# Kernel tuning notes

Measured on AMD Instinct MI355X. Metric: run time of the kernel, lower is better.

Reference implementation:

```python
import jax, jax.numpy as jnp
import numpy as np

CIN, COUT, KH, KW = 128, 256, 3, 3

def setup_inputs() -> dict:
    key = jax.random.key(0)
    kx, kw = jax.random.split(key)
    x = jax.random.normal(kx, (32, CIN, 56, 56), dtype=jnp.float32)
    # kaiming normal, fan_in mode, relu gain: std = sqrt(2 / fan_in)
    fan_in = CIN * KH * KW
    weight = jax.random.normal(kw, (COUT, CIN, KH, KW), dtype=jnp.float32) * jnp.sqrt(2.0 / fan_in)
    bias = jnp.zeros((COUT,), dtype=jnp.float32)
    return {"x": x, "weight": weight, "bias": bias}

def reference(x, weight, bias):
    # VALID 2D cross-correlation (matches torch conv semantics of the manual loop)
    y = jax.lax.conv_general_dilated(
        x, weight,
        window_strides=(1, 1),
        padding="VALID",
        dimension_numbers=("NCHW", "OIHW", "NCHW"),
    )
    return y + bias[None, :, None, None]
```

## Files before the change

### kernel.cpp

```cpp
#include <hip/hip_runtime.h>
#include <hip/hip_bf16.h>

#define CIN 128
#define COUT 256
#define H 56
#define W 56
#define OH 54
#define OW 54

typedef __attribute__((ext_vector_type(8))) short short8;
typedef __attribute__((ext_vector_type(4))) float floatx4;

typedef __attribute__((address_space(3))) unsigned int  lds_u32;
typedef const __attribute__((address_space(1))) unsigned int glb_u32;

static __device__ __forceinline__ unsigned short f2bf(float f) {
  unsigned int u = __builtin_bit_cast(unsigned int, f);
  u += 0x7fffu + ((u >> 16) & 1u);
  return (unsigned short)(u >> 16);
}

__global__ void repack_w(const float* __restrict__ w, unsigned short* __restrict__ w2) {
  int idx = blockIdx.x * 256 + threadIdx.x;
  if (idx >= COUT * CIN * 9) return;
  int kw = idx % 3, t1 = idx / 3;
  int kh = t1 % 3, t2 = t1 / 3;
  int ci = t2 % CIN;
  int co = t2 / CIN;
  int c8 = ci >> 3, j = ci & 7;
  w2[((((kh * 3 + kw) * 16 + c8) * COUT + co) * 8) + j] = f2bf(w[idx]);
}

__global__ __launch_bounds__(256) void repack_x(const float* __restrict__ x,
                                                unsigned short* __restrict__ xb) {
  __shared__ float xt[56][129];
  const int h = blockIdx.x;
  const int n = blockIdx.y;
  const float* src = x + (size_t)n * CIN * (H * W) + h * W;
  #pragma unroll
  for (int r = 0; r < 28; ++r) {
    int idx = r * 256 + threadIdx.x;
    int ci = idx / 56, iw = idx % 56;
    xt[iw][ci] = src[ci * (H * W) + iw];
  }
  __syncthreads();
  unsigned short* dst = xb + ((size_t)n * H + h) * 896 * 8;
  #pragma unroll
  for (int r = 0; r < 4; ++r) {
    int g = r * 256 + threadIdx.x;
    if (g < 896) {
      int iw = g >> 4, c16 = g & 15;
      short8 v;
      #pragma unroll
      for (int j = 0; j < 8; ++j)
        v[j] = (short)f2bf(xt[iw][c16 * 8 + j]);
      int gp = iw * 16 + (c16 ^ (iw & 7));
      *reinterpret_cast<short8*>(&dst[gp * 8]) = v;
    }
  }
}

__global__ __launch_bounds__(512, 2) void conv2(
    const unsigned short* __restrict__ xb, const unsigned short* __restrict__ w2,
    const float* __restrict__ bias, float* __restrict__ out) {
  __shared__ alignas(16) unsigned short xs[3744 * 8];

  const int f = blockIdx.x;
  const int swz = (f & 7) * 108 + (f >> 3);
  const int ohp = swz % 27;
  const int n   = swz / 27;
  const int oh0 = ohp * 2;
  const int tid = threadIdx.x;
  const int wid  = tid >> 6;
  const int lane = tid & 63;

  {
    const unsigned short* src = xb + ((size_t)n * H + oh0) * 896 * 8;
    #pragma unroll
    for (int i = 0; i < 7; ++i) {
      int idx = (wid * 7 + i) * 64;
      __builtin_amdgcn_global_load_lds(
          (glb_u32*)(src + (size_t)(idx + lane) * 8),
          (lds_u32*)(&xs[idx * 8]), 16, 0, 0);
    }
  }
  asm volatile("s_waitcnt vmcnt(0)" ::: "memory");
  __syncthreads();

  const int wm   = wid >> 1;
  const int wn   = wid & 1;
  const int l16  = lane & 15;
  const int cig  = lane >> 4;

  const int co_base = wm * 64;
  const int oh = oh0 + wn;

  const unsigned short* wbase = w2 + ((size_t)(cig * COUT + co_base + l16)) * 8;
  const int bwn = wn * 896 * 8;
  int ib[3], x7[3];
  #pragma unroll
  for (int kw = 0; kw < 3; ++kw) {
    ib[kw] = (l16 + kw) * 16 * 8;
    x7[kw] = (l16 + kw) & 7;
  }

  floatx4 acc[4][4];
  #pragma unroll
  for (int m = 0; m < 4; ++m)
    #pragma unroll
    for (int nr = 0; nr < 4; ++nr)
      acc[m][nr] = (floatx4){0.f, 0.f, 0.f, 0.f};

  short8 areg[2][4], breg[2][4];

#define STEP_LOAD(s, slot)                                                      \
  {                                                                             \
    const int kh_ = (s) / 12, ch_ = ((s) / 3) & 3, kw_ = (s) % 3;               \
    const unsigned short* wp_ =                                                 \
        wbase + (size_t)(((kh_ * 3 + kw_) * 16 + ch_ * 4) * COUT) * 8;          \
    areg[slot][0] = *reinterpret_cast<const short8*>(wp_);                      \
    areg[slot][1] = *reinterpret_cast<const short8*>(wp_ + 128);                \
    areg[slot][2] = *reinterpret_cast<const short8*>(wp_ + 256);                \
    areg[slot][3] = *reinterpret_cast<const short8*>(wp_ + 384);                \
    const int c16x_ = (ch_ * 4 + cig) ^ x7[kw_];                                \
    const int boff_ = bwn + kh_ * (896 * 8) + ib[kw_] + c16x_ * 8;              \
    breg[slot][0] = *reinterpret_cast<const short8*>(&xs[boff_]);               \
    breg[slot][1] = *reinterpret_cast<const short8*>(&xs[boff_ + 2048]);        \
    breg[slot][2] = *reinterpret_cast<const short8*>(&xs[boff_ + 4096]);        \
    breg[slot][3] = *reinterpret_cast<const short8*>(&xs[boff_ + 6144]);        \
  }

  STEP_LOAD(0, 0);
  #pragma unroll
  for (int s = 0; s < 36; ++s) {
    if (s < 35) STEP_LOAD(s + 1, (s + 1) & 1);
    __builtin_amdgcn_sched_barrier(0);
    __builtin_amdgcn_s_setprio(1);
    #pragma unroll
    for (int m = 0; m < 4; ++m)
      #pragma unroll
      for (int nr = 0; nr < 4; ++nr)
        acc[m][nr] = __builtin_amdgcn_mfma_f32_16x16x32_bf16(
            areg[s & 1][m], breg[s & 1][nr], acc[m][nr], 0, 0, 0);
    __builtin_amdgcn_s_setprio(0);
  }
#undef STEP_LOAD

  const int rowd = cig * 4;
  #pragma unroll
  for (int m = 0; m < 4; ++m) {
    #pragma unroll
    for (int reg = 0; reg < 4; ++reg) {
      int co = co_base + m * 16 + rowd + reg;
      float bv = bias[co];
      float* op = out + (((size_t)n * COUT + co) * OH + oh) * OW;
      #pragma unroll
      for (int nr = 0; nr < 4; ++nr) {
        int ow = nr * 16 + l16;
        if (ow < OW) op[ow] = acc[m][nr][reg] + bv;
      }
    }
  }
}

#define CSTR 136
#define IWP 66

__global__ __launch_bounds__(512, 4) void conv_fb(
    const float* __restrict__ x, const unsigned short* __restrict__ w2,
    const float* __restrict__ bias, float* __restrict__ out) {
  __shared__ alignas(16) unsigned short xsf[4 * IWP * CSTR];

  const int ohp = blockIdx.x;
  const int n   = blockIdx.y;
  const int oh0 = ohp * 2;
  const int tid = threadIdx.x;

  {
    short8 zz = {0, 0, 0, 0, 0, 0, 0, 0};
    for (int i = tid; i < 4 * 10 * 17; i += 512) {
      int r = i / 170, rem = i % 170;
      int iw = 56 + rem / 17, g = rem % 17;
      *reinterpret_cast<short8*>(&xsf[(r * IWP + iw) * CSTR + g * 8]) = zz;
    }
  }
  for (int s = tid; s < 3584; s += 512) {
    int iw = s % 56;
    int t  = s / 56;
    int c8 = t & 15, r = t >> 4;
    const float* xp = x + (size_t)n * CIN * (H * W) + (oh0 + r) * W + iw;
    short8 v;
    #pragma unroll
    for (int j = 0; j < 8; ++j)
      v[j] = (short)f2bf(xp[(size_t)(c8 * 8 + j) * (H * W)]);
    *reinterpret_cast<short8*>(&xsf[(r * IWP + iw) * CSTR + c8 * 8]) = v;
  }
  __syncthreads();

  const int wid  = tid >> 6;
  const int lane = tid & 63;
  const int wm   = wid >> 1;
  const int wn   = wid & 1;
  const int l16  = lane & 15;
  const int cig  = lane >> 4;

  const int co_base = wm * 64;
  const int oh = oh0 + wn;

  floatx4 acc[4][4];
  #pragma unroll
  for (int m = 0; m < 4; ++m)
    #pragma unroll
    for (int nr = 0; nr < 4; ++nr)
      acc[m][nr] = (floatx4){0.f, 0.f, 0.f, 0.f};

  for (int kh = 0; kh < 3; ++kh) {
    const int row = wn + kh;
    #pragma unroll
    for (int ch = 0; ch < 4; ++ch) {
      const int bbase = (row * IWP + l16) * CSTR + ch * 32 + cig * 8;
      #pragma unroll
      for (int kw = 0; kw < 3; ++kw) {
        const unsigned short* wp =
            w2 + ((size_t)(((kh * 3 + kw) * 16 + (ch * 4 + cig)) * COUT + co_base + l16)) * 8;
        short8 a[4];
        #pragma unroll
        for (int m = 0; m < 4; ++m)
          a[m] = *reinterpret_cast<const short8*>(wp + m * 16 * 8);
        short8 b[4];
        #pragma unroll
        for (int nr = 0; nr < 4; ++nr)
          b[nr] = *reinterpret_cast<const short8*>(&xsf[bbase + (nr * 16 + kw) * CSTR]);
        #pragma unroll
        for (int m = 0; m < 4; ++m)
          #pragma unroll
          for (int nr = 0; nr < 4; ++nr)
            acc[m][nr] = __builtin_amdgcn_mfma_f32_16x16x32_bf16(a[m], b[nr], acc[m][nr], 0, 0, 0);
      }
    }
  }

  const int rowd = cig * 4;
  #pragma unroll
  for (int m = 0; m < 4; ++m) {
    #pragma unroll
    for (int reg = 0; reg < 4; ++reg) {
      int co = co_base + m * 16 + rowd + reg;
      float bv = bias[co];
      float* op = out + (((size_t)n * COUT + co) * OH + oh) * OW;
      #pragma unroll
      for (int nr = 0; nr < 4; ++nr) {
        int ow = nr * 16 + l16;
        if (ow < OW) op[ow] = acc[m][nr][reg] + bv;
      }
    }
  }
}

extern "C" void kernel_launch(void* const* d_in, const int* in_sizes, int n_in,
                              void* d_out, int out_size, void* d_ws, size_t ws_size,
                              hipStream_t stream) {
  (void)in_sizes; (void)n_in; (void)out_size;
  const float* x    = (const float*)d_in[0];
  const float* w    = (const float*)d_in[1];
  const float* bias = (const float*)d_in[2];
  float* out = (float*)d_out;

  const size_t W2_BYTES = (size_t)9 * 16 * COUT * 8 * 2;
  const size_t XB_BYTES = (size_t)32 * H * 896 * 8 * 2;
  unsigned short* w2 = (unsigned short*)d_ws;

  repack_w<<<dim3((COUT * CIN * 9 + 255) / 256), dim3(256), 0, stream>>>(w, w2);

  if (ws_size >= W2_BYTES + XB_BYTES) {
    unsigned short* xb = (unsigned short*)((char*)d_ws + W2_BYTES);
    repack_x<<<dim3(56, 32), dim3(256), 0, stream>>>(x, xb);
    conv2<<<dim3(864), dim3(512), 0, stream>>>(xb, w2, bias, out);
  } else {
    conv_fb<<<dim3(27, 32), dim3(512), 0, stream>>>(x, w2, bias, out);
  }
}
```

Measured before the change: 92.60 us.

## Stage weights through LDS with a three-deep async pipeline in conv kernel

Weights are reordered so each of the 36 reduction steps reads one contiguous 16KB slab. The new conv kernel streams those slabs into a triple-buffered LDS area with async global-to-LDS loads, two steps ahead. Previously each wave loaded its weights straight from global memory into registers. The input-tile load is no longer waited on before the loop, so it overlaps the first weight stages, and bias is loaded up front. The cost is a block barrier every step, more LDS per block (possibly lower occupancy), and reliance on vmcnt ordering being correct.

Measured after the change: 138.4 us. 49.4% more time.

```diff
diff --git a/kernel.cpp b/kernel.cpp
--- a/kernel.cpp
+++ b/kernel.cpp
@@ -20,7 +20,179 @@
   return (unsigned short)(u >> 16);
 }
 
-__global__ void repack_w(const float* __restrict__ w, unsigned short* __restrict__ w2) {
+__global__ void repack_w(const float* __restrict__ w, unsigned short* __restrict__ w3) {
+  int idx = blockIdx.x * 256 + threadIdx.x;
+  if (idx >= COUT * CIN * 9) return;
+  int kw = idx % 3, t1 = idx / 3;
+  int kh = t1 % 3, t2 = t1 / 3;
+  int ci = t2 % CIN;
+  int co = t2 / CIN;
+  int c8 = ci >> 3, j = ci & 7;
+  int ch = c8 >> 2, g = c8 & 3;
+  int s = kh * 12 + ch * 3 + kw;
+  w3[(((s * 4 + g) * COUT + co) * 8) + j] = f2bf(w[idx]);
+}
+
+__global__ __launch_bounds__(256) void repack_x(const float* __restrict__ x,
+                                                unsigned short* __restrict__ xb) {
+  __shared__ float xt[56][129];
+  const int h = blockIdx.x;
+  const int n = blockIdx.y;
+  const float* src = x + (size_t)n * CIN * (H * W) + h * W;
+  #pragma unroll
+  for (int r = 0; r < 28; ++r) {
+    int idx = r * 256 + threadIdx.x;
+    int ci = idx / 56, iw = idx % 56;
+    xt[iw][ci] = src[ci * (H * W) + iw];
+  }
+  __syncthreads();
+  unsigned short* dst = xb + ((size_t)n * H + h) * 896 * 8;
+  #pragma unroll
+  for (int r = 0; r < 4; ++r) {
+    int g = r * 256 + threadIdx.x;
+    if (g < 896) {
+      int iw = g >> 4, c16 = g & 15;
+      short8 v;
+      #pragma unroll
+      for (int j = 0; j < 8; ++j)
+        v[j] = (short)f2bf(xt[iw][c16 * 8 + j]);
+      int gp = iw * 16 + (c16 ^ (iw & 7));
+      *reinterpret_cast<short8*>(&dst[gp * 8]) = v;
+    }
+  }
+}
+
+__global__ __launch_bounds__(512, 2) void conv4(
+    const unsigned short* __restrict__ xb, const unsigned short* __restrict__ w3,
+    const float* __restrict__ bias, float* __restrict__ out) {
+  __shared__ alignas(16) unsigned short xs[3744 * 8];
+  __shared__ alignas(16) unsigned short abuf[3][1024 * 8];
+
+  const int f = blockIdx.x;
+  const int swz = (f & 7) * 108 + (f >> 3);
+  const int ohp = swz % 27;
+  const int n   = swz / 27;
+  const int oh0 = ohp * 2;
+  const int tid = threadIdx.x;
+  const int wid  = tid >> 6;
+  const int lane = tid & 63;
+
+  const int wm   = wid >> 1;
+  const int wn   = wid & 1;
+  const int l16  = lane & 15;
+  const int cig  = lane >> 4;
+  const int co_base = wm * 64;
+  const int oh = oh0 + wn;
+  const int rowd = cig * 4;
+
+  float bv[4][4];
+  #pragma unroll
+  for (int m = 0; m < 4; ++m)
+    #pragma unroll
+    for (int reg = 0; reg < 4; ++reg)
+      bv[m][reg] = bias[co_base + m * 16 + rowd + reg];
+
+  {
+    const unsigned short* src = xb + ((size_t)n * H + oh0) * 896 * 8;
+    #pragma unroll
+    for (int i = 0; i < 7; ++i) {
+      int idx = (wid * 7 + i) * 64;
+      __builtin_amdgcn_global_load_lds(
+          (glb_u32*)(src + (size_t)(idx + lane) * 8),
+          (lds_u32*)(&xs[idx * 8]), 16, 0, 0);
+    }
+  }
+
+#define ASTAGE(t)                                                               \
+  {                                                                             \
+    const unsigned short* asrc_ = w3 + (size_t)(t) * 8192;                      \
+    unsigned short* adst_ = &abuf[(t) % 3][0];                                  \
+    const int b0_ = (wid * 2) * 64;                                             \
+    const int b1_ = (wid * 2 + 1) * 64;                                         \
+    __builtin_amdgcn_global_load_lds((glb_u32*)(asrc_ + (size_t)(b0_ + lane) * 8), \
+                                     (lds_u32*)(adst_ + (size_t)b0_ * 8), 16, 0, 0); \
+    __builtin_amdgcn_global_load_lds((glb_u32*)(asrc_ + (size_t)(b1_ + lane) * 8), \
+                                     (lds_u32*)(adst_ + (size_t)b1_ * 8), 16, 0, 0); \
+  }
+
+  ASTAGE(0);
+  ASTAGE(1);
+  asm volatile("s_waitcnt vmcnt(2)" ::: "memory");
+  __builtin_amdgcn_s_barrier();
+  __builtin_amdgcn_sched_barrier(0);
+
+  const int bwn = wn * 896 * 8;
+  int ib[3], x7[3];
+  #pragma unroll
+  for (int kw = 0; kw < 3; ++kw) {
+    ib[kw] = (l16 + kw) * 128;
+    x7[kw] = (l16 + kw) & 7;
+  }
+  const int aoff = (cig * 256 + co_base + l16) * 8;
+
+  floatx4 acc[4][4];
+  #pragma unroll
+  for (int m = 0; m < 4; ++m)
+    #pragma unroll
+    for (int nr = 0; nr < 4; ++nr)
+      acc[m][nr] = (floatx4){0.f, 0.f, 0.f, 0.f};
+
+  #pragma unroll
+  for (int t = 0; t < 36; ++t) {
+    if (t + 2 < 36) ASTAGE(t + 2);
+
+    const int kh = t / 12, ch = (t / 3) & 3, kw = t % 3;
+    short8 a[4], b[4];
+    const unsigned short* ab = &abuf[t % 3][aoff];
+    a[0] = *reinterpret_cast<const short8*>(ab);
+    a[1] = *reinterpret_cast<const short8*>(ab + 128);
+    a[2] = *reinterpret_cast<const short8*>(ab + 256);
+    a[3] = *reinterpret_cast<const short8*>(ab + 384);
+    const int c16x = (ch * 4 + cig) ^ x7[kw];
+    const int boff = bwn + kh * (896 * 8) + ib[kw] + c16x * 8;
+    b[0] = *reinterpret_cast<const short8*>(&xs[boff]);
+    b[1] = *reinterpret_cast<const short8*>(&xs[boff + 2048]);
+    b[2] = *reinterpret_cast<const short8*>(&xs[boff + 4096]);
+    b[3] = *reinterpret_cast<const short8*>(&xs[boff + 6144]);
+
+    __builtin_amdgcn_sched_barrier(0);
+    __builtin_amdgcn_s_setprio(1);
+    #pragma unroll
+    for (int m = 0; m < 4; ++m)
+      #pragma unroll
+      for (int nr = 0; nr < 4; ++nr)
+        acc[m][nr] = __builtin_amdgcn_mfma_f32_16x16x32_bf16(a[m], b[nr], acc[m][nr], 0, 0, 0);
+    __builtin_amdgcn_s_setprio(0);
+    __builtin_amdgcn_sched_barrier(0);
+
+    if (t < 34)       asm volatile("s_waitcnt vmcnt(2)" ::: "memory");
+    else if (t == 34) asm volatile("s_waitcnt vmcnt(0)" ::: "memory");
+    if (t < 35) {
+      __builtin_amdgcn_s_barrier();
+      __builtin_amdgcn_sched_barrier(0);
+    }
+  }
+#undef ASTAGE
+
+  #pragma unroll
+  for (int m = 0; m < 4; ++m) {
+    #pragma unroll
+    for (int reg = 0; reg < 4; ++reg) {
+      int co = co_base + m * 16 + rowd + reg;
+      float* op = out + (((size_t)n * COUT + co) * OH + oh) * OW;
+      #pragma unroll
+      for (int nr = 0; nr < 4; ++nr) {
+        int ow = nr * 16 + l16;
+        if (ow < OW) op[ow] = acc[m][nr][reg] + bv[m][reg];
+      }
+    }
+  }
+}
+
+#define CSTR 136
+#define IWP 66
+
+__global__ void repack_w_fb(const float* __restrict__ w, unsigned short* __restrict__ w2) {
   int idx = blockIdx.x * 256 + threadIdx.x;
   if (idx >= COUT * CIN * 9) return;
   int kw = idx % 3, t1 = idx / 3;
@@ -30,141 +202,6 @@
   int c8 = ci >> 3, j = ci & 7;
   w2[((((kh * 3 + kw) * 16 + c8) * COUT + co) * 8) + j] = f2bf(w[idx]);
 }
-
-__global__ __launch_bounds__(256) void repack_x(const float* __restrict__ x,
-                                                unsigned short* __restrict__ xb) {
-  __shared__ float xt[56][129];
-  const int h = blockIdx.x;
-  const int n = blockIdx.y;
-  const float* src = x + (size_t)n * CIN * (H * W) + h * W;
-  #pragma unroll
-  for (int r = 0; r < 28; ++r) {
-    int idx = r * 256 + threadIdx.x;
-    int ci = idx / 56, iw = idx % 56;
-    xt[iw][ci] = src[ci * (H * W) + iw];
-  }
-  __syncthreads();
-  unsigned short* dst = xb + ((size_t)n * H + h) * 896 * 8;
-  #pragma unroll
-  for (int r = 0; r < 4; ++r) {
-    int g = r * 256 + threadIdx.x;
-    if (g < 896) {
-      int iw = g >> 4, c16 = g & 15;
-      short8 v;
-      #pragma unroll
-      for (int j = 0; j < 8; ++j)
-        v[j] = (short)f2bf(xt[iw][c16 * 8 + j]);
-      int gp = iw * 16 + (c16 ^ (iw & 7));
-      *reinterpret_cast<short8*>(&dst[gp * 8]) = v;
-    }
-  }
-}
-
-__global__ __launch_bounds__(512, 2) void conv2(
-    const unsigned short* __restrict__ xb, const unsigned short* __restrict__ w2,
-    const float* __restrict__ bias, float* __restrict__ out) {
-  __shared__ alignas(16) unsigned short xs[3744 * 8];
-
-  const int f = blockIdx.x;
-  const int swz = (f & 7) * 108 + (f >> 3);
-  const int ohp = swz % 27;
-  const int n   = swz / 27;
-  const int oh0 = ohp * 2;
-  const int tid = threadIdx.x;
-  const int wid  = tid >> 6;
-  const int lane = tid & 63;
-
-  {
-    const unsigned short* src = xb + ((size_t)n * H + oh0) * 896 * 8;
-    #pragma unroll
-    for (int i = 0; i < 7; ++i) {
-      int idx = (wid * 7 + i) * 64;
-      __builtin_amdgcn_global_load_lds(
-          (glb_u32*)(src + (size_t)(idx + lane) * 8),
-          (lds_u32*)(&xs[idx * 8]), 16, 0, 0);
-    }
-  }
-  asm volatile("s_waitcnt vmcnt(0)" ::: "memory");
-  __syncthreads();
-
-  const int wm   = wid >> 1;
-  const int wn   = wid & 1;
-  const int l16  = lane & 15;
-  const int cig  = lane >> 4;
-
-  const int co_base = wm * 64;
-  const int oh = oh0 + wn;
-
-  const unsigned short* wbase = w2 + ((size_t)(cig * COUT + co_base + l16)) * 8;
-  const int bwn = wn * 896 * 8;
-  int ib[3], x7[3];
-  #pragma unroll
-  for (int kw = 0; kw < 3; ++kw) {
-    ib[kw] = (l16 + kw) * 16 * 8;
-    x7[kw] = (l16 + kw) & 7;
-  }
-
-  floatx4 acc[4][4];
-  #pragma unroll
-  for (int m = 0; m < 4; ++m)
-    #pragma unroll
-    for (int nr = 0; nr < 4; ++nr)
-      acc[m][nr] = (floatx4){0.f, 0.f, 0.f, 0.f};
-
-  short8 areg[2][4], breg[2][4];
-
-#define STEP_LOAD(s, slot)                                                      \
-  {                                                                             \
-    const int kh_ = (s) / 12, ch_ = ((s) / 3) & 3, kw_ = (s) % 3;               \
-    const unsigned short* wp_ =                                                 \
-        wbase + (size_t)(((kh_ * 3 + kw_) * 16 + ch_ * 4) * COUT) * 8;          \
-    areg[slot][0] = *reinterpret_cast<const short8*>(wp_);                      \
-    areg[slot][1] = *reinterpret_cast<const short8*>(wp_ + 128);                \
-    areg[slot][2] = *reinterpret_cast<const short8*>(wp_ + 256);                \
-    areg[slot][3] = *reinterpret_cast<const short8*>(wp_ + 384);                \
-    const int c16x_ = (ch_ * 4 + cig) ^ x7[kw_];                                \
-    const int boff_ = bwn + kh_ * (896 * 8) + ib[kw_] + c16x_ * 8;              \
-    breg[slot][0] = *reinterpret_cast<const short8*>(&xs[boff_]);               \
-    breg[slot][1] = *reinterpret_cast<const short8*>(&xs[boff_ + 2048]);        \
-    breg[slot][2] = *reinterpret_cast<const short8*>(&xs[boff_ + 4096]);        \
-    breg[slot][3] = *reinterpret_cast<const short8*>(&xs[boff_ + 6144]);        \
-  }
-
-  STEP_LOAD(0, 0);
-  #pragma unroll
-  for (int s = 0; s < 36; ++s) {
-    if (s < 35) STEP_LOAD(s + 1, (s + 1) & 1);
-    __builtin_amdgcn_sched_barrier(0);
-    __builtin_amdgcn_s_setprio(1);
-    #pragma unroll
-    for (int m = 0; m < 4; ++m)
-      #pragma unroll
-      for (int nr = 0; nr < 4; ++nr)
-        acc[m][nr] = __builtin_amdgcn_mfma_f32_16x16x32_bf16(
-            areg[s & 1][m], breg[s & 1][nr], acc[m][nr], 0, 0, 0);
-    __builtin_amdgcn_s_setprio(0);
-  }
-#undef STEP_LOAD
-
-  const int rowd = cig * 4;
-  #pragma unroll
-  for (int m = 0; m < 4; ++m) {
-    #pragma unroll
-    for (int reg = 0; reg < 4; ++reg) {
-      int co = co_base + m * 16 + rowd + reg;
-      float bv = bias[co];
-      float* op = out + (((size_t)n * COUT + co) * OH + oh) * OW;
-      #pragma unroll
-      for (int nr = 0; nr < 4; ++nr) {
-        int ow = nr * 16 + l16;
-        if (ow < OW) op[ow] = acc[m][nr][reg] + bv;
-      }
-    }
-  }
-}
-
-#define CSTR 136
-#define IWP 66
 
 __global__ __launch_bounds__(512, 4) void conv_fb(
     const float* __restrict__ x, const unsigned short* __restrict__ w2,
@@ -246,12 +283,12 @@
     #pragma unroll
     for (int reg = 0; reg < 4; ++reg) {
       int co = co_base + m * 16 + rowd + reg;
-      float bv = bias[co];
+      float bvv = bias[co];
       float* op = out + (((size_t)n * COUT + co) * OH + oh) * OW;
       #pragma unroll
       for (int nr = 0; nr < 4; ++nr) {
         int ow = nr * 16 + l16;
-        if (ow < OW) op[ow] = acc[m][nr][reg] + bv;
+        if (ow < OW) op[ow] = acc[m][nr][reg] + bvv;
       }
     }
   }
@@ -266,17 +303,17 @@
   const float* bias = (const float*)d_in[2];
   float* out = (float*)d_out;
 
-  const size_t W2_BYTES = (size_t)9 * 16 * COUT * 8 * 2;
+  const size_t W3_BYTES = (size_t)36 * 4 * COUT * 8 * 2;
   const size_t XB_BYTES = (size_t)32 * H * 896 * 8 * 2;
-  unsigned short* w2 = (unsigned short*)d_ws;
-
-  repack_w<<<dim3((COUT * CIN * 9 + 255) / 256), dim3(256), 0, stream>>>(w, w2);
-
-  if (ws_size >= W2_BYTES + XB_BYTES) {
-    unsigned short* xb = (unsigned short*)((char*)d_ws + W2_BYTES);
-    repack_x<<<dim3(56, 32), dim3(256), 0, stream>>>(x, xb);
-    conv2<<<dim3(864), dim3(512), 0, stream>>>(xb, w2, bias, out);
+  unsigned short* wrep = (unsigned short*)d_ws;
+
+  if (ws_size >= W3_BYTES + XB_BYTES) {
+    unsigned short* xbuf = (unsigned short*)((char*)d_ws + W3_BYTES);
+    repack_w<<<dim3((COUT * CIN * 9 + 255) / 256), dim3(256), 0, stream>>>(w, wrep);
+    repack_x<<<dim3(56, 32), dim3(256), 0, stream>>>(x, xbuf);
+    conv4<<<dim3(864), dim3(512), 0, stream>>>(xbuf, wrep, bias, out);
   } else {
-    conv_fb<<<dim3(27, 32), dim3(512), 0, stream>>>(x, w2, bias, out);
-  }
-}
+    repack_w_fb<<<dim3((COUT * CIN * 9 + 255) / 256), dim3(256), 0, stream>>>(w, wrep);
+    conv_fb<<<dim3(27, 32), dim3(512), 0, stream>>>(x, wrep, bias, out);
+  }
+}
```

## Shrink conv tile to one output row per 256-thread block

Applied to the files above, without the earlier changes.

Each conv block now covers a single output row with 4 waves (each owning 64 output channels), down from two rows with 8 waves, so the grid doubles to 1728 blocks and LDS per block shrinks to 3 input rows. This targets higher occupancy and finer load balancing, at the cost of loading each input row into LDS three times instead of two-row tiles sharing overlap. The explicit register double-buffering of weight and LDS loads is removed in favour of compiler scheduling, and bias is loaded before the main loop. Input loads near the end of the buffer are clamped to stay in bounds.

Measured after the change: 93.04 us. About the same (+0.5%).

```diff
diff --git a/kernel.cpp b/kernel.cpp
--- a/kernel.cpp
+++ b/kernel.cpp
@@ -60,50 +60,48 @@
   }
 }
 
-__global__ __launch_bounds__(512, 2) void conv2(
+__global__ __launch_bounds__(256, 3) void conv6(
     const unsigned short* __restrict__ xb, const unsigned short* __restrict__ w2,
     const float* __restrict__ bias, float* __restrict__ out) {
-  __shared__ alignas(16) unsigned short xs[3744 * 8];
+  __shared__ alignas(16) unsigned short xs[2880 * 8];
 
   const int f = blockIdx.x;
-  const int swz = (f & 7) * 108 + (f >> 3);
-  const int ohp = swz % 27;
-  const int n   = swz / 27;
-  const int oh0 = ohp * 2;
-  const int tid = threadIdx.x;
+  const int swz = (f & 7) * 216 + (f >> 3);
+  const int oh = swz % 54;
+  const int n  = swz / 54;
+  const int tid  = threadIdx.x;
   const int wid  = tid >> 6;
   const int lane = tid & 63;
+  const int l16  = lane & 15;
+  const int cig  = lane >> 4;
+  const int co_base = wid * 64;
+  const int rowd = cig * 4;
+
+  float bv[4][4];
+  #pragma unroll
+  for (int m = 0; m < 4; ++m)
+    #pragma unroll
+    for (int reg = 0; reg < 4; ++reg)
+      bv[m][reg] = bias[co_base + m * 16 + rowd + reg];
 
   {
-    const unsigned short* src = xb + ((size_t)n * H + oh0) * 896 * 8;
-    #pragma unroll
-    for (int i = 0; i < 7; ++i) {
-      int idx = (wid * 7 + i) * 64;
-      __builtin_amdgcn_global_load_lds(
-          (glb_u32*)(src + (size_t)(idx + lane) * 8),
-          (lds_u32*)(&xs[idx * 8]), 16, 0, 0);
+    const size_t gbase = ((size_t)n * H + oh) * 896;
+    const size_t gmax  = (size_t)32 * H * 896 - 64;
+    #pragma unroll
+    for (int i = 0; i < 12; ++i) {
+      int c = i * 4 + wid;
+      if (c < 45) {
+        size_t sg = gbase + (size_t)c * 64;
+        if (sg > gmax) sg = gmax;
+        __builtin_amdgcn_global_load_lds(
+            (glb_u32*)(xb + (sg + lane) * 8),
+            (lds_u32*)(&xs[(size_t)c * 64 * 8]), 16, 0, 0);
+      }
     }
   }
   asm volatile("s_waitcnt vmcnt(0)" ::: "memory");
   __syncthreads();
 
-  const int wm   = wid >> 1;
-  const int wn   = wid & 1;
-  const int l16  = lane & 15;
-  const int cig  = lane >> 4;
-
-  const int co_base = wm * 64;
-  const int oh = oh0 + wn;
-
-  const unsigned short* wbase = w2 + ((size_t)(cig * COUT + co_base + l16)) * 8;
-  const int bwn = wn * 896 * 8;
-  int ib[3], x7[3];
-  #pragma unroll
-  for (int kw = 0; kw < 3; ++kw) {
-    ib[kw] = (l16 + kw) * 16 * 8;
-    x7[kw] = (l16 + kw) & 7;
-  }
-
   floatx4 acc[4][4];
   #pragma unroll
   for (int m = 0; m < 4; ++m)
@@ -111,53 +109,42 @@
     for (int nr = 0; nr < 4; ++nr)
       acc[m][nr] = (floatx4){0.f, 0.f, 0.f, 0.f};
 
-  short8 areg[2][4], breg[2][4];
-
-#define STEP_LOAD(s, slot)                                                      \
-  {                                                                             \
-    const int kh_ = (s) / 12, ch_ = ((s) / 3) & 3, kw_ = (s) % 3;               \
-    const unsigned short* wp_ =                                                 \
-        wbase + (size_t)(((kh_ * 3 + kw_) * 16 + ch_ * 4) * COUT) * 8;          \
-    areg[slot][0] = *reinterpret_cast<const short8*>(wp_);                      \
-    areg[slot][1] = *reinterpret_cast<const short8*>(wp_ + 128);                \
-    areg[slot][2] = *reinterpret_cast<const short8*>(wp_ + 256);                \
-    areg[slot][3] = *reinterpret_cast<const short8*>(wp_ + 384);                \
-    const int c16x_ = (ch_ * 4 + cig) ^ x7[kw_];                                \
-    const int boff_ = bwn + kh_ * (896 * 8) + ib[kw_] + c16x_ * 8;              \
-    breg[slot][0] = *reinterpret_cast<const short8*>(&xs[boff_]);               \
-    breg[slot][1] = *reinterpret_cast<const short8*>(&xs[boff_ + 2048]);        \
-    breg[slot][2] = *reinterpret_cast<const short8*>(&xs[boff_ + 4096]);        \
-    breg[slot][3] = *reinterpret_cast<const short8*>(&xs[boff_ + 6144]);        \
-  }
-
-  STEP_LOAD(0, 0);
   #pragma unroll
   for (int s = 0; s < 36; ++s) {
-    if (s < 35) STEP_LOAD(s + 1, (s + 1) & 1);
-    __builtin_amdgcn_sched_barrier(0);
+    const int kh = s / 12, ch = (s / 3) & 3, kw = s % 3;
+    const unsigned short* wp =
+        w2 + ((size_t)(((kh * 3 + kw) * 16 + (ch * 4 + cig)) * COUT + co_base + l16)) * 8;
+    short8 a[4];
+    #pragma unroll
+    for (int m = 0; m < 4; ++m)
+      a[m] = *reinterpret_cast<const short8*>(wp + m * 128);
+    const int iwl = l16 + kw;
+    const int c16x = (ch * 4 + cig) ^ (iwl & 7);
+    const int boff = (kh * 896 + iwl * 16 + c16x) * 8;
+    short8 b[4];
+    #pragma unroll
+    for (int nr = 0; nr < 4; ++nr)
+      b[nr] = *reinterpret_cast<const short8*>(&xs[boff + nr * 2048]);
+
     __builtin_amdgcn_s_setprio(1);
     #pragma unroll
     for (int m = 0; m < 4; ++m)
       #pragma unroll
       for (int nr = 0; nr < 4; ++nr)
-        acc[m][nr] = __builtin_amdgcn_mfma_f32_16x16x32_bf16(
-            areg[s & 1][m], breg[s & 1][nr], acc[m][nr], 0, 0, 0);
+        acc[m][nr] = __builtin_amdgcn_mfma_f32_16x16x32_bf16(a[m], b[nr], acc[m][nr], 0, 0, 0);
     __builtin_amdgcn_s_setprio(0);
   }
-#undef STEP_LOAD
-
-  const int rowd = cig * 4;
+
   #pragma unroll
   for (int m = 0; m < 4; ++m) {
     #pragma unroll
     for (int reg = 0; reg < 4; ++reg) {
       int co = co_base + m * 16 + rowd + reg;
-      float bv = bias[co];
       float* op = out + (((size_t)n * COUT + co) * OH + oh) * OW;
       #pragma unroll
       for (int nr = 0; nr < 4; ++nr) {
         int ow = nr * 16 + l16;
-        if (ow < OW) op[ow] = acc[m][nr][reg] + bv;
+        if (ow < OW) op[ow] = acc[m][nr][reg] + bv[m][reg];
       }
     }
   }
@@ -246,12 +233,12 @@
     #pragma unroll
     for (int reg = 0; reg < 4; ++reg) {
       int co = co_base + m * 16 + rowd + reg;
-      float bv = bias[co];
+      float bvv = bias[co];
       float* op = out + (((size_t)n * COUT + co) * OH + oh) * OW;
       #pragma unroll
       for (int nr = 0; nr < 4; ++nr) {
         int ow = nr * 16 + l16;
-        if (ow < OW) op[ow] = acc[m][nr][reg] + bv;
+        if (ow < OW) op[ow] = acc[m][nr][reg] + bvv;
       }
     }
   }
@@ -275,7 +262,7 @@
   if (ws_size >= W2_BYTES + XB_BYTES) {
     unsigned short* xb = (unsigned short*)((char*)d_ws + W2_BYTES);
     repack_x<<<dim3(56, 32), dim3(256), 0, stream>>>(x, xb);
-    conv2<<<dim3(864), dim3(512), 0, stream>>>(xb, w2, bias, out);
+    conv6<<<dim3(1728), dim3(256), 0, stream>>>(xb, w2, bias, out);
   } else {
     conv_fb<<<dim3(27, 32), dim3(512), 0, stream>>>(x, w2, bias, out);
   }
```
